# Optimization experiments

Measured on AMD Instinct MI355X. Metric: run time of the kernel, lower is better.

## Reference

```python
import jax, jax.numpy as jnp
import numpy as np

B, S, D = 2, 1024, 7168
H, HD, RD, QL = 64, 128, 64, 1536
EPS = 1e-6
SOFTMAX_SCALE = HD ** (-0.5)


def _rope_interleave(x, cos, sin):
    """Interleaved RoPE (pairs x[2i], x[2i+1]); x: [T, n, RD], cos/sin: [T, RD]."""
    x1 = x[..., 0::2]
    x2 = x[..., 1::2]
    c = cos[:, None, 0::2]
    s = sin[:, None, 0::2]
    o1 = x1 * c - x2 * s
    o2 = x2 * c + x1 * s
    return jnp.stack([o1, o2], axis=-1).reshape(x.shape)


def setup_inputs() -> dict:
    key = jax.random.key(0)
    ks = jax.random.split(key, 8)
    x = jax.random.normal(ks[0], (B, S, D), dtype=jnp.float32) * 0.02
    qr = jax.random.normal(ks[1], (B * S, QL), dtype=jnp.float32) * 0.02
    # real interleaved-RoPE cos/sin tables, tiled over batch
    pos = jnp.arange(S, dtype=jnp.float32)
    inv_freq = 1.0 / (10000.0 ** (jnp.arange(0, RD, 2, dtype=jnp.float32) / RD))
    freqs = pos[:, None] * inv_freq[None, :]                      # [S, RD/2]
    cos = jnp.repeat(jnp.cos(freqs), 2, axis=-1)                  # [S, RD]
    sin = jnp.repeat(jnp.sin(freqs), 2, axis=-1)
    cos = jnp.tile(cos, (B, 1))                                   # [B*S, RD]
    sin = jnp.tile(sin, (B, 1))
    wq_b_w = jax.random.normal(ks[2], (QL, H * HD), dtype=jnp.float32) * (QL ** -0.5)
    wk_w = jax.random.normal(ks[3], (D, HD), dtype=jnp.float32) * (D ** -0.5)
    wproj_w = jax.random.normal(ks[4], (D, H), dtype=jnp.float32) * (D ** -0.5)
    ln_gamma = jnp.ones((HD,), dtype=jnp.float32)
    ln_beta = jnp.ones((HD,), dtype=jnp.float32)  # module inits bias to ones
    return {"x": x, "qr": qr, "cos": cos, "sin": sin, "wq_b_w": wq_b_w,
            "wk_w": wk_w, "wproj_w": wproj_w, "ln_gamma": ln_gamma, "ln_beta": ln_beta}


def reference(x, qr, cos, sin, wq_b_w, wk_w, wproj_w, ln_gamma, ln_beta):
    b, s, d = x.shape
    t = b * s
    xf = x.reshape(t, d)
    # ---- query path: low-rank up-proj, split rope/nope, interleaved RoPE ----
    q = (qr @ wq_b_w).reshape(t, H, HD)
    q_pe, q_nope = q[..., :RD], q[..., RD:]
    q_pe = _rope_interleave(q_pe, cos, sin)
    q = jnp.concatenate([q_pe, q_nope], axis=-1).reshape(b, s, H, HD)
    # ---- per-head gating weights ----
    w = (xf @ wproj_w).reshape(b, s, H)
    # ---- key path: project, LayerNorm, RoPE on rope slice ----
    kp = xf @ wk_w                                                # [T, HD]
    mu = jnp.mean(kp, axis=-1, keepdims=True)
    var = jnp.mean(jnp.square(kp - mu), axis=-1, keepdims=True)
    kn = (kp - mu) * jax.lax.rsqrt(var + EPS) * ln_gamma + ln_beta
    k_pe, k_nope = kn[..., :RD], kn[..., RD:]
    k_pe = _rope_interleave(k_pe[:, None, :], cos, sin)[:, 0]
    k = jnp.concatenate([k_pe, k_nope], axis=-1).reshape(b, s, HD)
    # ---- lightning-indexer scores: weighted ReLU(q.k) summed over heads ----
    logits = jnp.einsum("bqhd,bkd->bqhk", q, k)                   # [B,S,H,S]
    scores = SOFTMAX_SCALE * jnp.einsum("bqh,bqhk->bqk", w, jax.nn.relu(logits))
    return scores
```

## Files before the change

kernel.cpp:

```cpp
#include <hip/hip_runtime.h>

typedef unsigned short u16;
typedef unsigned int   u32;

typedef __bf16 bf16x8 __attribute__((ext_vector_type(8)));
typedef float  f32x4  __attribute__((ext_vector_type(4)));

__device__ __forceinline__ float bf2f(u16 u){ u32 x = ((u32)u) << 16; return __builtin_bit_cast(float, x); }
__device__ __forceinline__ u16 f2bf(float f){
  u32 u = __builtin_bit_cast(u32, f);
  u32 r = (u + 0x7FFFu + ((u >> 16) & 1u)) >> 16;
  return (u16)r;
}
__device__ __forceinline__ u32 pk2bf(float a, float b){
  u32 ua = __builtin_bit_cast(u32, a) + 0x8000u;
  u32 ub = __builtin_bit_cast(u32, b) + 0x8000u;
  return __builtin_amdgcn_perm(ub, ua, 0x07060302u);
}
__device__ __forceinline__ void glds16(const void* g, void* l){
  __builtin_amdgcn_global_load_lds((const __attribute__((address_space(1))) void*)g,
                                   (__attribute__((address_space(3))) void*)l, 16, 0, 0);
}

__global__ __launch_bounds__(256) void transpose_f32_bf16_v(const float* __restrict__ src,
                                                            u16* __restrict__ dst, int R, int C){
  __shared__ u16 T[64 * 72];
  int c0 = blockIdx.x * 64, r0 = blockIdx.y * 64;
  int tr  = threadIdx.x >> 3;
  int tc8 = (threadIdx.x & 7) * 8;
  #pragma unroll
  for (int it = 0; it < 2; ++it){
    int rr = tr + it * 32;
    const float* sp = src + (size_t)(r0 + rr) * C + c0 + tc8;
    float4 f0 = *(const float4*)sp, f1 = *(const float4*)(sp + 4);
    u16 v[8] = { f2bf(f0.x), f2bf(f0.y), f2bf(f0.z), f2bf(f0.w),
                 f2bf(f1.x), f2bf(f1.y), f2bf(f1.z), f2bf(f1.w) };
    #pragma unroll
    for (int j = 0; j < 8; ++j) T[(tc8 + j) * 72 + rr] = v[j];
  }
  __syncthreads();
  int tcw = threadIdx.x >> 3;
  int tr8 = (threadIdx.x & 7) * 8;
  #pragma unroll
  for (int it = 0; it < 2; ++it){
    int cc = tcw + it * 32;
    *(uint4*)(dst + (size_t)(c0 + cc) * R + r0 + tr8) = *(const uint4*)&T[cc * 72 + tr8];
  }
}

__global__ __launch_bounds__(256) void cvt_f32_bf16(const float* __restrict__ src,
                                                    u16* __restrict__ dst){
  size_t i = ((size_t)blockIdx.x * 256 + threadIdx.x) * 8;
  const float4* a4 = (const float4*)(src + i);
  float4 f0 = a4[0], f1 = a4[1];
  u32 w[4] = { pk2bf(f0.x, f0.y), pk2bf(f0.z, f0.w), pk2bf(f1.x, f1.y), pk2bf(f1.z, f1.w) };
  *(uint4*)(dst + i) = *(const uint4*)w;
}

__global__ __launch_bounds__(256) void proj_splitk(const float* __restrict__ X,
    const u16* __restrict__ BT, float* __restrict__ P){
  constexpr int Kf = 7168;
  const int s = blockIdx.x, m0 = blockIdx.y * 64;
  const int kbase = s * 448;
  __shared__ u16 As[2 * 64 * 36];
  __shared__ u16 Bs[2 * 192 * 32];
  const int tid = threadIdx.x, wave = tid >> 6, lane = tid & 63;
  const int row = lane & 15, quad = lane >> 4;
  const int wm = (wave & 1) * 32, wn = (wave >> 1) * 96;

  const f32x4 zero = {0.f, 0.f, 0.f, 0.f};
  f32x4 acc[2][6];
  #pragma unroll
  for (int mt = 0; mt < 2; ++mt)
    #pragma unroll
    for (int nt = 0; nt < 6; ++nt) acc[mt][nt] = zero;

  for (int kb = 0; kb < 7; ++kb) {
    int k0 = kbase + kb * 64;
    #pragma unroll
    for (int c = 0; c < 6; ++c) {
      int chunk = wave * 6 + c;
      int kc = chunk / 12, rem = chunk % 12;
      int r = rem * 16 + (lane >> 2), col = (lane & 3) * 8;
      glds16(BT + (size_t)r * Kf + k0 + kc * 32 + col, (void*)&Bs[chunk * 512]);
    }
    #pragma unroll
    for (int c = 0; c < 2; ++c) {
      int idx = tid + c * 256;
      int r = idx >> 3, kf = (idx & 7) * 8;
      const float4* ap = (const float4*)(X + (size_t)(m0 + r) * Kf + k0 + kf);
      float4 f0 = ap[0], f1 = ap[1];
      u32 w[4] = { pk2bf(f0.x, f0.y), pk2bf(f0.z, f0.w), pk2bf(f1.x, f1.y), pk2bf(f1.z, f1.w) };
      *(uint4*)&As[(kf >> 5) * 2304 + r * 36 + (kf & 31)] = *(const uint4*)w;
    }
    __syncthreads();
    #pragma unroll
    for (int ks = 0; ks < 2; ++ks) {
      bf16x8 af[2], bfr[6];
      #pragma unroll
      for (int mt = 0; mt < 2; ++mt) af[mt] = *(const bf16x8*)&As[ks * 2304 + (wm + mt * 16 + row) * 36 + quad * 8];
      #pragma unroll
      for (int nt = 0; nt < 6; ++nt) bfr[nt] = *(const bf16x8*)&Bs[ks * 6144 + (wn + nt * 16 + row) * 32 + quad * 8];
      #pragma unroll
      for (int mt = 0; mt < 2; ++mt)
        #pragma unroll
        for (int nt = 0; nt < 6; ++nt)
          acc[mt][nt] = __builtin_amdgcn_mfma_f32_16x16x32_bf16(af[mt], bfr[nt], acc[mt][nt], 0, 0, 0);
    }
    __syncthreads();
  }
  #pragma unroll
  for (int mt = 0; mt < 2; ++mt)
    #pragma unroll
    for (int nt = 0; nt < 6; ++nt)
      #pragma unroll
      for (int r = 0; r < 4; ++r) {
        int rr = m0 + wm + mt * 16 + quad * 4 + r;
        int cc = wn + nt * 16 + row;
        P[((size_t)s * 2048 + rr) * 192 + cc] = acc[mt][nt][r];
      }
}

__global__ __launch_bounds__(64) void reduce_lnrope(const float* __restrict__ P,
    const float* __restrict__ cosb, const float* __restrict__ sinb,
    const float* __restrict__ gam, const float* __restrict__ bet,
    u16* __restrict__ Kout, float* __restrict__ WoutT){
  int tok = blockIdx.x, lane = threadIdx.x;
  float v0 = 0.f, v1 = 0.f, w = 0.f;
  #pragma unroll
  for (int s = 0; s < 16; ++s) {
    const float* p = P + ((size_t)s * 2048 + tok) * 192;
    v0 += p[2 * lane]; v1 += p[2 * lane + 1]; w += p[128 + lane];
  }
  WoutT[(size_t)lane * 2048 + tok] = w;
  float sm = v0 + v1;
  #pragma unroll
  for (int m = 1; m < 64; m <<= 1) sm += __shfl_xor(sm, m);
  float mu = sm * (1.f / 128.f);
  float d0 = v0 - mu, d1 = v1 - mu;
  float sq = d0 * d0 + d1 * d1;
  #pragma unroll
  for (int m = 1; m < 64; m <<= 1) sq += __shfl_xor(sq, m);
  float rs = rsqrtf(sq * (1.f / 128.f) + 1e-6f);
  float kn0 = d0 * rs * gam[2 * lane]     + bet[2 * lane];
  float kn1 = d1 * rs * gam[2 * lane + 1] + bet[2 * lane + 1];
  float o0 = kn0, o1 = kn1;
  if (lane < 32) {
    float c  = cosb[tok * 64 + 2 * lane];
    float sn = sinb[tok * 64 + 2 * lane];
    o0 = kn0 * c - kn1 * sn;
    o1 = kn1 * c + kn0 * sn;
  }
  Kout[tok * 128 + 2 * lane]     = f2bf(o0);
  Kout[tok * 128 + 2 * lane + 1] = f2bf(o1);
}

template<bool AGLDS>
__global__ __launch_bounds__(256) void qgemm(const void* __restrict__ Aptr,
    const u16* __restrict__ BT, const float* __restrict__ cosb,
    const float* __restrict__ sinb, u16* __restrict__ Qout){
  constexpr int K = 1536, N = 8192;
  __shared__ u16 As[2 * 128 * 32];
  __shared__ u16 Bs[2 * 128 * 32];
  const int tid = threadIdx.x, wave = tid >> 6, lane = tid & 63;
  const int row = lane & 15, quad = lane >> 4;
  const int wm = (wave >> 1) * 64, wn = (wave & 1) * 64;
  const int m0 = blockIdx.y * 128, n0 = blockIdx.x * 128;

  const f32x4 zero = {0.f, 0.f, 0.f, 0.f};
  f32x4 acc[4][4];
  #pragma unroll
  for (int mt = 0; mt < 4; ++mt)
    #pragma unroll
    for (int nt = 0; nt < 4; ++nt) acc[mt][nt] = zero;

  for (int k0 = 0; k0 < K; k0 += 64) {
    #pragma unroll
    for (int c = 0; c < 4; ++c) {
      int chunk = wave * 4 + c;
      int kc = chunk >> 3, rg = chunk & 7;
      int r = rg * 16 + (lane >> 2), col = kc * 32 + (lane & 3) * 8;
      glds16(BT + (size_t)(n0 + r) * K + k0 + col, (void*)&Bs[chunk * 512]);
    }
    if (AGLDS) {
      #pragma unroll
      for (int c = 0; c < 4; ++c) {
        int chunk = wave * 4 + c;
        int kc = chunk >> 3, rg = chunk & 7;
        int r = rg * 16 + (lane >> 2), col = kc * 32 + (lane & 3) * 8;
        glds16((const u16*)Aptr + (size_t)(m0 + r) * K + k0 + col, (void*)&As[chunk * 512]);
      }
    } else {
      #pragma unroll
      for (int c = 0; c < 4; ++c) {
        int idx = tid + c * 256;
        int r = idx >> 3, kf = (idx & 7) * 8;
        const float4* ap = (const float4*)((const float*)Aptr + (size_t)(m0 + r) * K + k0 + kf);
        float4 f0 = ap[0], f1 = ap[1];
        u32 w[4] = { pk2bf(f0.x, f0.y), pk2bf(f0.z, f0.w), pk2bf(f1.x, f1.y), pk2bf(f1.z, f1.w) };
        *(uint4*)&As[(kf >> 5) * 4096 + r * 32 + (kf & 31)] = *(const uint4*)w;
      }
    }
    __syncthreads();
    #pragma unroll
    for (int kk = 0; kk < 2; ++kk) {
      bf16x8 af[4], bfr[4];
      #pragma unroll
      for (int mt = 0; mt < 4; ++mt) af[mt]  = *(const bf16x8*)&As[kk * 4096 + (wm + mt * 16 + row) * 32 + quad * 8];
      #pragma unroll
      for (int nt = 0; nt < 4; ++nt) bfr[nt] = *(const bf16x8*)&Bs[kk * 4096 + (wn + nt * 16 + row) * 32 + quad * 8];
      #pragma unroll
      for (int mt = 0; mt < 4; ++mt)
        #pragma unroll
        for (int nt = 0; nt < 4; ++nt)
          acc[mt][nt] = __builtin_amdgcn_mfma_f32_16x16x32_bf16(af[mt], bfr[nt], acc[mt][nt], 0, 0, 0);
    }
    __syncthreads();
  }

  const bool roped = (wn == 0);
  #pragma unroll
  for (int mt = 0; mt < 4; ++mt)
    #pragma unroll
    for (int nt = 0; nt < 4; ++nt)
      #pragma unroll
      for (int r = 0; r < 4; ++r) {
        int rr = m0 + wm + mt * 16 + quad * 4 + r;
        int cc = n0 + wn + nt * 16 + row;
        float v = acc[mt][nt][r];
        float o = v;
        if (roped) {
          int hd = (wn + nt * 16 + row) & 127;
          float c = cosb[rr * 64 + hd];
          float s = sinb[rr * 64 + hd];
          float vo = __shfl_xor(v, 1);
          o = (cc & 1) ? (v * c + vo * s) : (v * c - vo * s);
        }
        Qout[(size_t)rr * N + cc] = f2bf(o);
      }
}

__global__ __launch_bounds__(256) void attn_kernel(const u16* __restrict__ Q,
    const u16* __restrict__ Kb, const float* __restrict__ WT, float* __restrict__ out){
  int blk = blockIdx.x;
  int x = blk & 7, kt = (blk >> 3) & 7, hs = (blk >> 6) & 1, g4 = (blk >> 7) & 3;
  int p = x + 8 * g4;
  int b = p >> 4, qt = p & 15;
  int q0 = qt * 64, k0 = kt * 128;

  const int tid = threadIdx.x, wave = tid >> 6, lane = tid & 63;
  const int row = lane & 15, quad = lane >> 4;
  const int wm = (wave >> 1) * 32;
  const int wn = (wave & 1) * 64;

  __shared__ u16 Sh[2][16384];
  __shared__ float Ws[32 * 64];

  #pragma unroll
  for (int c = 0; c < 8; ++c) {
    int g = wave * 8 + c;
    int rr = g * 4 + (lane >> 4), col = (lane & 15) * 8;
    glds16(Kb + (size_t)(b * 1024 + k0 + rr) * 128 + col, (void*)&Sh[0][g * 512]);
  }
  {
    int hl = tid >> 3, qq = (tid & 7) * 8;
    const float* srcw = WT + (size_t)(hs * 32 + hl) * 2048 + b * 1024 + q0 + qq;
    *(float4*)&Ws[hl * 64 + qq]     = *(const float4*)srcw;
    *(float4*)&Ws[hl * 64 + qq + 4] = *(const float4*)(srcw + 4);
  }
  __syncthreads();

  bf16x8 bfr[4][4];
  #pragma unroll
  for (int ks = 0; ks < 4; ++ks)
    #pragma unroll
    for (int nt = 0; nt < 4; ++nt)
      bfr[ks][nt] = *(const bf16x8*)&Sh[0][(wn + nt * 16 + row) * 128 + ks * 32 + quad * 8];
  __syncthreads();

  const u16* Qbase = Q + (size_t)(b * 1024 + q0) * 8192;
  auto stage = [&](int half, int pairIdx){
    int h0 = hs * 32 + pairIdx * 2;
    #pragma unroll
    for (int c = 0; c < 8; ++c) {
      int g = wave * 8 + c;
      int hsub = g >> 4, rem = g & 15;
      int kc = rem >> 2, rg = rem & 3;
      glds16(Qbase + (size_t)(rg * 16 + (lane >> 2)) * 8192 + (h0 + hsub) * 128 + kc * 32 + (lane & 3) * 8,
             (void*)&Sh[half][hsub * 8192 + rem * 512]);
    }
  };

  const f32x4 zero = {0.f, 0.f, 0.f, 0.f};
  f32x4 sacc[2][4];
  #pragma unroll
  for (int mt = 0; mt < 2; ++mt)
    #pragma unroll
    for (int nt = 0; nt < 4; ++nt) sacc[mt][nt] = zero;

  stage(0, 0);
  for (int hp = 0; hp < 16; ++hp) {
    __syncthreads();
    if (hp < 15) stage((hp + 1) & 1, hp + 1);
    const u16* S = Sh[hp & 1];
    #pragma unroll
    for (int hsub = 0; hsub < 2; ++hsub) {
      f32x4 lg[2][4];
      #pragma unroll
      for (int mt = 0; mt < 2; ++mt)
        #pragma unroll
        for (int nt = 0; nt < 4; ++nt) lg[mt][nt] = zero;
      #pragma unroll
      for (int ks = 0; ks < 4; ++ks) {
        bf16x8 af0 = *(const bf16x8*)&S[hsub * 8192 + ks * 2048 + (wm +      row) * 32 + quad * 8];
        bf16x8 af1 = *(const bf16x8*)&S[hsub * 8192 + ks * 2048 + (wm + 16 + row) * 32 + quad * 8];
        #pragma unroll
        for (int nt = 0; nt < 4; ++nt) {
          lg[0][nt] = __builtin_amdgcn_mfma_f32_16x16x32_bf16(af0, bfr[ks][nt], lg[0][nt], 0, 0, 0);
          lg[1][nt] = __builtin_amdgcn_mfma_f32_16x16x32_bf16(af1, bfr[ks][nt], lg[1][nt], 0, 0, 0);
        }
      }
      int hl = hp * 2 + hsub;
      f32x4 w0 = *(const f32x4*)&Ws[hl * 64 + wm +      quad * 4];
      f32x4 w1 = *(const f32x4*)&Ws[hl * 64 + wm + 16 + quad * 4];
      #pragma unroll
      for (int nt = 0; nt < 4; ++nt)
        #pragma unroll
        for (int r = 0; r < 4; ++r) {
          sacc[0][nt][r] += w0[r] * fmaxf(lg[0][nt][r], 0.f);
          sacc[1][nt][r] += w1[r] * fmaxf(lg[1][nt][r], 0.f);
        }
    }
  }

  const float scale = 0.088388347648318447f;
  #pragma unroll
  for (int mt = 0; mt < 2; ++mt)
    #pragma unroll
    for (int nt = 0; nt < 4; ++nt)
      #pragma unroll
      for (int r = 0; r < 4; ++r) {
        int qq = q0 + wm + mt * 16 + quad * 4 + r;
        int kk = k0 + wn + nt * 16 + row;
        unsafeAtomicAdd(&out[((size_t)b << 20) + (size_t)qq * 1024 + kk], scale * sacc[mt][nt][r]);
      }
}

extern "C" void kernel_launch(void* const* d_in, const int* in_sizes, int n_in,
                              void* d_out, int out_size, void* d_ws, size_t ws_size,
                              hipStream_t stream) {
  const float* x    = (const float*)d_in[0];
  const float* qr   = (const float*)d_in[1];
  const float* cosb = (const float*)d_in[2];
  const float* sinb = (const float*)d_in[3];
  const float* wq   = (const float*)d_in[4];
  const float* wk   = (const float*)d_in[5];
  const float* wp   = (const float*)d_in[6];
  const float* gam  = (const float*)d_in[7];
  const float* bet  = (const float*)d_in[8];
  float* out = (float*)d_out;

  char* ws = (char*)d_ws;
  float* P    = (float*)(ws + 0);
  u16*   wqT  = (u16*)(ws + 0);
  u16*   wkwpT= (u16*)(ws + 25165824);
  float* WT   = (float*)(ws + 27918336);
  u16*   Kbf  = (u16*)(ws + 28442624);
  u16*   Qbf  = (u16*)(ws + 28966912);
  const size_t QRB_OFF = 62521344;
  u16*   qrb  = (u16*)(ws + QRB_OFF);
  const bool big_ws = (ws_size >= (size_t)68812800);

  (void)in_sizes; (void)n_in;

  hipMemsetAsync(d_out, 0, (size_t)out_size * 4, stream);

  transpose_f32_bf16_v<<<dim3(2, 112), 256, 0, stream>>>(wk, wkwpT,              7168, 128);
  transpose_f32_bf16_v<<<dim3(1, 112), 256, 0, stream>>>(wp, wkwpT + 128 * 7168, 7168, 64);

  proj_splitk<<<dim3(16, 32), 256, 0, stream>>>(x, wkwpT, P);
  reduce_lnrope<<<2048, 64, 0, stream>>>(P, cosb, sinb, gam, bet, Kbf, WT);

  transpose_f32_bf16_v<<<dim3(128, 24), 256, 0, stream>>>(wq, wqT, 1536, 8192);

  if (big_ws) {
    cvt_f32_bf16<<<1536, 256, 0, stream>>>(qr, qrb);
    qgemm<true><<<dim3(64, 16), 256, 0, stream>>>(qrb, wqT, cosb, sinb, Qbf);
  } else {
    qgemm<false><<<dim3(64, 16), 256, 0, stream>>>(qr, wqT, cosb, sinb, Qbf);
  }

  attn_kernel<<<512, 256, 0, stream>>>(Qbf, Kbf, WT, out);
}
```

Measured before the change: 327.8 us.

## Add 256x128-tile triple-buffered Q GEMM with direct-to-LDS loads

Adds a new Q up-projection GEMM kernel with 512 threads and 256x128 output tiles. It uses a three-stage LDS ring fed by global_load_lds, XOR-swizzled LDS reads, explicit vmcnt waits and raised wave priority around the MFMA block. The RoPE epilogue is kept, and the bf16 input path now uses this kernel. The aim is more data reuse per tile and better overlap of loads with MFMA work, at the cost of more LDS per block and fewer blocks.

Result: no change. 322.3 us (-1.7%).

```diff
diff --git a/kernel.cpp b/kernel.cpp
--- a/kernel.cpp
+++ b/kernel.cpp
@@ -20,6 +20,11 @@
 __device__ __forceinline__ void glds16(const void* g, void* l){
   __builtin_amdgcn_global_load_lds((const __attribute__((address_space(1))) void*)g,
                                    (__attribute__((address_space(3))) void*)l, 16, 0, 0);
+}
+__device__ __forceinline__ void hard_barrier(){
+  asm volatile("" ::: "memory");
+  __builtin_amdgcn_s_barrier();
+  asm volatile("" ::: "memory");
 }
 
 __global__ __launch_bounds__(256) void transpose_f32_bf16_v(const float* __restrict__ src,
@@ -240,6 +245,117 @@
       }
 }
 
+__global__ __launch_bounds__(512, 2) void qgemm256(const u16* __restrict__ A,
+    const u16* __restrict__ BT, const float* __restrict__ cosb,
+    const float* __restrict__ sinb, u16* __restrict__ Qout){
+  constexpr int K = 1536, N = 8192, NT = 24;
+  __shared__ __align__(16) u16 Asb[3][16384];
+  __shared__ __align__(16) u16 Bsb[3][8192];
+  const int tid = threadIdx.x, wave = tid >> 6, lane = tid & 63;
+  const int lrow = lane & 15, quad = lane >> 4;
+  const int wr = wave >> 1, wc = wave & 1;
+  const int m0 = blockIdx.y * 256, n0 = blockIdx.x * 128;
+
+  const int colb = ((lane & 7) << 4) ^ ((lane & 8) << 3) ^ ((lane & 16) << 1);
+  const int cole = colb >> 1;
+  const int sub  = lane >> 3;
+  const u16* pa[4];
+  const u16* pb[2];
+  #pragma unroll
+  for (int c = 0; c < 4; ++c) {
+    int g = wave * 4 + c;
+    pa[c] = A + (size_t)(m0 + g * 8 + sub) * K + cole;
+  }
+  #pragma unroll
+  for (int c = 0; c < 2; ++c) {
+    int g = wave * 2 + c;
+    pb[c] = BT + (size_t)(n0 + g * 8 + sub) * K + cole;
+  }
+
+  auto stage = [&](int t, int buf){
+    int koff = t * 64;
+    #pragma unroll
+    for (int c = 0; c < 4; ++c)
+      glds16(pa[c] + koff, (void*)&Asb[buf][(wave * 4 + c) * 512]);
+    #pragma unroll
+    for (int c = 0; c < 2; ++c)
+      glds16(pb[c] + koff, (void*)&Bsb[buf][(wave * 2 + c) * 512]);
+  };
+
+  const int swz  = ((lrow & 1) << 6) | ((lrow & 2) << 4);
+  const int aob  = (wr * 64 + lrow) * 128 + quad * 16;
+  const int bob  = (wc * 64 + lrow) * 128 + quad * 16;
+
+  const f32x4 zero = {0.f, 0.f, 0.f, 0.f};
+  f32x4 acc[4][4];
+  #pragma unroll
+  for (int mt = 0; mt < 4; ++mt)
+    #pragma unroll
+    for (int nt = 0; nt < 4; ++nt) acc[mt][nt] = zero;
+
+  auto compute = [&](int buf){
+    const char* Ab = (const char*)Asb[buf];
+    const char* Bb = (const char*)Bsb[buf];
+    bf16x8 af[2][4], bfr[2][4];
+    #pragma unroll
+    for (int kk = 0; kk < 2; ++kk) {
+      #pragma unroll
+      for (int mt = 0; mt < 4; ++mt)
+        af[kk][mt]  = *(const bf16x8*)(Ab + ((aob + mt * 2048 + kk * 64) ^ swz));
+      #pragma unroll
+      for (int nt = 0; nt < 4; ++nt)
+        bfr[kk][nt] = *(const bf16x8*)(Bb + ((bob + nt * 2048 + kk * 64) ^ swz));
+    }
+    __builtin_amdgcn_s_setprio(1);
+    #pragma unroll
+    for (int kk = 0; kk < 2; ++kk)
+      #pragma unroll
+      for (int mt = 0; mt < 4; ++mt)
+        #pragma unroll
+        for (int nt = 0; nt < 4; ++nt)
+          acc[mt][nt] = __builtin_amdgcn_mfma_f32_16x16x32_bf16(af[kk][mt], bfr[kk][nt], acc[mt][nt], 0, 0, 0);
+    __builtin_amdgcn_s_setprio(0);
+  };
+
+  stage(0, 0);
+  stage(1, 1);
+  asm volatile("s_waitcnt vmcnt(6)" ::: "memory");
+  hard_barrier();
+
+  #pragma unroll
+  for (int t = 0; t < NT; ++t) {
+    if (t + 2 < NT) stage(t + 2, (t + 2) % 3);
+    compute(t % 3);
+    if (t < NT - 1) {
+      if (t <= NT - 3) { asm volatile("s_waitcnt vmcnt(6)" ::: "memory"); }
+      else             { asm volatile("s_waitcnt vmcnt(0)" ::: "memory"); }
+      hard_barrier();
+      __builtin_amdgcn_sched_barrier(0);
+    }
+  }
+
+  const bool roped = (wc == 0);
+  #pragma unroll
+  for (int mt = 0; mt < 4; ++mt)
+    #pragma unroll
+    for (int nt = 0; nt < 4; ++nt)
+      #pragma unroll
+      for (int r = 0; r < 4; ++r) {
+        int rr = m0 + wr * 64 + mt * 16 + quad * 4 + r;
+        int cc = n0 + wc * 64 + nt * 16 + lrow;
+        float v = acc[mt][nt][r];
+        float o = v;
+        if (roped) {
+          int hd = nt * 16 + lrow;
+          float c = cosb[rr * 64 + hd];
+          float s = sinb[rr * 64 + hd];
+          float vo = __shfl_xor(v, 1);
+          o = (cc & 1) ? (v * c + vo * s) : (v * c - vo * s);
+        }
+        Qout[(size_t)rr * N + cc] = f2bf(o);
+      }
+}
+
 __global__ __launch_bounds__(256) void attn_kernel(const u16* __restrict__ Q,
     const u16* __restrict__ Kb, const float* __restrict__ WT, float* __restrict__ out){
   int blk = blockIdx.x;
@@ -385,7 +501,7 @@
 
   if (big_ws) {
     cvt_f32_bf16<<<1536, 256, 0, stream>>>(qr, qrb);
-    qgemm<true><<<dim3(64, 16), 256, 0, stream>>>(qrb, wqT, cosb, sinb, Qbf);
+    qgemm256<<<dim3(64, 8), 512, 0, stream>>>(qrb, wqT, cosb, sinb, Qbf);
   } else {
     qgemm<false><<<dim3(64, 16), 256, 0, stream>>>(qr, wqT, cosb, sinb, Qbf);
   }
```
